# Kernel tuning notes

Hardware: AMD Instinct MI355X
Metric: run time of the kernel (lower is better)

## Reference

```python
import jax, jax.numpy as jnp
import numpy as np

B = 512

def conv2d(x, w, b, stride, pad):
    y = jax.lax.conv_general_dilated(x, w, (stride, stride), [(pad, pad), (pad, pad)],
                                     dimension_numbers=('NCHW', 'OIHW', 'NCHW'))
    return y + b[None, :, None, None]

def maxpool(x, k, s, pad):
    return jax.lax.reduce_window(x, -jnp.inf, jax.lax.max,
                                 (1, 1, k, k), (1, 1, s, s),
                                 [(0, 0), (0, 0), (pad, pad), (pad, pad)])

def squash(s, axis=-1):
    sq = jnp.sum(s * s, axis=axis, keepdims=True)
    return (sq / (1.0 + sq)) * s / jnp.sqrt(sq + 1e-8)

def setup_inputs() -> dict:
    key = jax.random.key(0)
    ks = jax.random.split(key, 24)
    def w(k, shape, fan_in):
        return jax.random.normal(k, shape, dtype=jnp.float32) * np.float32(np.sqrt(2.0 / fan_in))
    inp = {}
    inp['x']  = jax.random.normal(ks[0], (B, 1, 28, 28), dtype=jnp.float32)
    inp['w1'] = w(ks[1], (96, 1, 3, 3), 1 * 9);     inp['b1'] = jnp.zeros((96,), jnp.float32)
    inp['w2'] = w(ks[2], (256, 96, 3, 3), 96 * 9);  inp['b2'] = jnp.zeros((256,), jnp.float32)
    inp['w3'] = w(ks[3], (384, 256, 3, 3), 256 * 9);inp['b3'] = jnp.zeros((384,), jnp.float32)
    inp['w4'] = w(ks[4], (384, 384, 3, 3), 384 * 9);inp['b4'] = jnp.zeros((384,), jnp.float32)
    inp['w5'] = w(ks[5], (256, 384, 3, 3), 384 * 9);inp['b5'] = jnp.zeros((256,), jnp.float32)
    # PrimaryCaps conv: 256 -> 32 caps * 8 dim = 256 channels, k2 s1 p0
    inp['wp'] = w(ks[6], (256, 256, 2, 2), 256 * 4);inp['bp'] = jnp.zeros((256,), jnp.float32)
    # DenseCapsule routing weight [out_caps=10, in_caps=512, out_dim=16, in_dim=8]
    inp['Wr'] = jax.random.normal(ks[7], (10, 512, 16, 8), dtype=jnp.float32) * 0.01
    inp['fw1'] = w(ks[8], (4096, 160), 160);   inp['fb1'] = jnp.zeros((4096,), jnp.float32)
    inp['fw2'] = w(ks[9], (4096, 4096), 4096); inp['fb2'] = jnp.zeros((4096,), jnp.float32)
    inp['fw3'] = w(ks[10], (10, 4096), 4096);  inp['fb3'] = jnp.zeros((10,), jnp.float32)
    return inp

def reference(x, w1, b1, w2, b2, w3, b3, w4, b4, w5, b5, wp, bp, Wr,
              fw1, fb1, fw2, fb2, fw3, fb3):
    # AlexNet-style conv stack (eval mode; dropout = identity)
    h = jax.nn.relu(conv2d(x, w1, b1, 1, 1))   # [B,96,28,28]
    h = maxpool(h, 3, 2, 1)                    # [B,96,14,14]
    h = jax.nn.relu(conv2d(h, w2, b2, 1, 1))   # [B,256,14,14]
    h = maxpool(h, 3, 2, 1)                    # [B,256,7,7]
    h = jax.nn.relu(conv2d(h, w3, b3, 1, 1))   # [B,384,7,7]
    h = jax.nn.relu(conv2d(h, w4, b4, 1, 1))   # [B,384,7,7]
    h = jax.nn.relu(conv2d(h, w5, b5, 1, 1))   # [B,256,7,7]
    h = maxpool(h, 3, 1, 0)                    # [B,256,5,5]
    # PrimaryCaps: conv k2 -> [B,256,4,4] -> [B,512,8] -> squash
    p = conv2d(h, wp, bp, 1, 0)                # [B,256,4,4]
    u = p.reshape(p.shape[0], -1, 8)           # [B,512,8]
    u = squash(u)
    # DenseCapsule dynamic routing (3 iterations)
    x_hat = jnp.einsum('oivd,bid->boiv', Wr, u)     # [B,10,512,16]
    x_hat_d = jax.lax.stop_gradient(x_hat)
    b = jnp.zeros(x_hat.shape[:3], x_hat.dtype)     # [B,10,512]
    routings = 3
    for i in range(routings):
        c = jax.nn.softmax(b, axis=1)
        if i == routings - 1:
            v = squash(jnp.einsum('boi,boiv->bov', c, x_hat))
        else:
            v = squash(jnp.einsum('boi,boiv->bov', c, x_hat_d))
            b = b + jnp.einsum('bov,boiv->boi', v, x_hat_d)
    # Flatten + FC head
    f = v.reshape(v.shape[0], -1)                   # [B,160]
    f = jax.nn.relu(f @ fw1.T + fb1)
    f = jax.nn.relu(f @ fw2.T + fb2)
    return f @ fw3.T + fb3                          # [B,10]
```

## Files before the change

### kernel.cpp

```cpp
#include <hip/hip_runtime.h>
#include <math.h>


#define BATCH 512

typedef _Float16 half8  __attribute__((ext_vector_type(8)));
typedef _Float16 half4v __attribute__((ext_vector_type(4)));
typedef float   float4v __attribute__((ext_vector_type(4)));

__global__ __launch_bounds__(256) void split_kernel(
    const float* __restrict__ src, _Float16* __restrict__ hi,
    _Float16* __restrict__ lo, int n)
{
    int idx = blockIdx.x * 256 + threadIdx.x;
    if (idx >= n) return;
    float v = src[idx];
    _Float16 h = (_Float16)v;
    hi[idx] = h;
    lo[idx] = (_Float16)((v - (float)h) * 2048.0f);
}

__global__ __launch_bounds__(256) void wsplit_nhwc_kernel(
    const float* __restrict__ src, _Float16* __restrict__ hi,
    _Float16* __restrict__ lo, int IC, int KK, int n)
{
    int idx = blockIdx.x * 256 + threadIdx.x;
    if (idx >= n) return;
    int ic   = idx % IC;  int t1 = idx / IC;
    int khkw = t1 % KK;   int oc = t1 / KK;
    float v = src[((size_t)(oc * IC + ic)) * KK + khkw];
    _Float16 h = (_Float16)v;
    hi[idx] = h;
    lo[idx] = (_Float16)((v - (float)h) * 2048.0f);
}

__global__ __launch_bounds__(256) void conv1_pool_nhwc(
    const float* __restrict__ x, const float* __restrict__ w1,
    const float* __restrict__ b1, _Float16* __restrict__ oh_,
    _Float16* __restrict__ ol_)
{
    int idx = blockIdx.x * 256 + threadIdx.x;
    if (idx >= 512 * 14 * 14 * 96) return;
    int oc = idx % 96; int t1 = idx / 96;
    int ow = t1 % 14;  int t2 = t1 / 14;
    int oh = t2 % 14;  int n  = t2 / 14;
    const float* xi = x + n * 784;
    float w[9];
#pragma unroll
    for (int i = 0; i < 9; ++i) w[i] = w1[oc * 9 + i];
    float bias = b1[oc];
    float best = -3.4e38f;
#pragma unroll
    for (int dy = 0; dy < 3; ++dy) {
        int ph = oh * 2 - 1 + dy;
        if ((unsigned)ph >= 28u) continue;
#pragma unroll
        for (int dx = 0; dx < 3; ++dx) {
            int pw = ow * 2 - 1 + dx;
            if ((unsigned)pw >= 28u) continue;
            float s = bias;
#pragma unroll
            for (int ky = 0; ky < 3; ++ky) {
                int iy = ph - 1 + ky;
                if ((unsigned)iy >= 28u) continue;
#pragma unroll
                for (int kx = 0; kx < 3; ++kx) {
                    int ix = pw - 1 + kx;
                    if ((unsigned)ix >= 28u) continue;
                    s = fmaf(w[ky * 3 + kx], xi[iy * 28 + ix], s);
                }
            }
            s = fmaxf(s, 0.f);
            best = fmaxf(best, s);
        }
    }
    _Float16 h = (_Float16)best;
    oh_[idx] = h;
    ol_[idx] = (_Float16)((best - (float)h) * 2048.0f);
}

template<int NB, int C, int H, int W, int OH, int OW, int KS, int STR, int PADP>
__global__ __launch_bounds__(256) void maxpool_nhwc_split(
    const float* __restrict__ in, _Float16* __restrict__ po,
    _Float16* __restrict__ pl)
{
    constexpr int TOTAL = NB * OH * OW * C;
    int idx = blockIdx.x * 256 + threadIdx.x;
    if (idx >= TOTAL) return;
    int c  = idx % C;  int t1 = idx / C;
    int ow = t1 % OW;  int t2 = t1 / OW;
    int oh = t2 % OH;  int n  = t2 / OH;
    const float* ip = in + (size_t)n * (H * W * C) + c;
    float best = -3.4e38f;
#pragma unroll
    for (int dy = 0; dy < KS; ++dy) {
        int ih = oh * STR - PADP + dy;
        if ((unsigned)ih >= (unsigned)H) continue;
#pragma unroll
        for (int dx = 0; dx < KS; ++dx) {
            int iw = ow * STR - PADP + dx;
            if ((unsigned)iw >= (unsigned)W) continue;
            best = fmaxf(best, ip[(size_t)(ih * W + iw) * C]);
        }
    }
    _Float16 h = (_Float16)best;
    po[idx] = h;
    pl[idx] = (_Float16)((best - (float)h) * 2048.0f);
}

template<int IC, int H, int W, int KH, int PAD, int OC, int OUTMODE>
__global__ __launch_bounds__(256, 3) void conv_nhwc_f16x3(
    const _Float16* __restrict__ inh, const _Float16* __restrict__ inl,
    const _Float16* __restrict__ whi, const _Float16* __restrict__ wlo,
    const float* __restrict__ bias,
    float* __restrict__ outf, _Float16* __restrict__ outh,
    _Float16* __restrict__ outl, int n_base)
{
    constexpr int OH  = H + 2 * PAD - KH + 1;
    constexpr int OW  = W + 2 * PAD - KH + 1;
    constexpr int OHW = OH * OW;
    constexpr int K   = IC * KH * KH;
    constexpr int RS  = 40;
    static_assert(IC % 32 == 0, "K-step must sit inside one (kh,kw)");

    const int t    = threadIdx.x;
    const int lane = t & 63;
    const int wid  = t >> 6;
    const int wm   = (wid >> 1) << 6;
    const int wn   = (wid & 1) << 5;
    const int l15  = lane & 15;
    const int quad = lane >> 4;

    __shared__ __align__(16) _Float16 Ah[128 * RS];
    __shared__ __align__(16) _Float16 Al[128 * RS];
    __shared__ __align__(16) _Float16 Bh[64 * RS];
    __shared__ __align__(16) _Float16 Bl[64 * RS];

    const int n0 = blockIdx.x << 6;
    const int m0 = blockIdx.y << 7;

    float4v acc1[8], acc2[8];
#pragma unroll
    for (int i = 0; i < 8; ++i) {
        acc1[i] = (float4v)(0.f);
        acc2[i] = (float4v)(0.f);
    }

    const int am = t >> 1;
    const int ak = (t & 1) << 4;
    const _Float16* wh_p = whi + (size_t)(m0 + am) * K + ak;
    const _Float16* wl_p = wlo + (size_t)(m0 + am) * K + ak;

    const int n_u  = t & 63;
    const int k8   = ((t >> 6) & 3) << 3;
    const int gn_u = n_base + n0 + n_u;
    const int b_u  = gn_u / OHW;
    const int p_u  = gn_u - b_u * OHW;
    const int oh_u = p_u / OW;
    const int ow_u = p_u - oh_u * OW;
    const _Float16* inbh = inh + (size_t)b_u * (H * W * IC);
    const _Float16* inbl = inl + (size_t)b_u * (H * W * IC);

    int khkw = 0, icb = 0;
    for (int kb = 0; kb < K; kb += 32) {
        *(half8*)&Ah[am * RS + ak]     = *(const half8*)(wh_p + kb);
        *(half8*)&Ah[am * RS + ak + 8] = *(const half8*)(wh_p + kb + 8);
        *(half8*)&Al[am * RS + ak]     = *(const half8*)(wl_p + kb);
        *(half8*)&Al[am * RS + ak + 8] = *(const half8*)(wl_p + kb + 8);
        {
            const int kh = khkw / KH;
            const int kw = khkw - kh * KH;
            const int ih = oh_u + kh - PAD;
            const int iw = ow_u + kw - PAD;
            half8 hv = (half8)(_Float16)0.f;
            half8 lv = (half8)(_Float16)0.f;
            if ((unsigned)ih < (unsigned)H && (unsigned)iw < (unsigned)W) {
                const size_t off = (size_t)(ih * W + iw) * IC + icb + k8;
                hv = *(const half8*)(inbh + off);
                lv = *(const half8*)(inbl + off);
            }
            *(half8*)&Bh[n_u * RS + k8] = hv;
            *(half8*)&Bl[n_u * RS + k8] = lv;
        }
        __syncthreads();
        half8 ah[4], al[4], bh[2], bl[2];
#pragma unroll
        for (int i = 0; i < 4; ++i) {
            int ar = wm + i * 16 + l15;
            ah[i] = *(const half8*)&Ah[ar * RS + quad * 8];
            al[i] = *(const half8*)&Al[ar * RS + quad * 8];
        }
#pragma unroll
        for (int i = 0; i < 2; ++i) {
            int br = wn + i * 16 + l15;
            bh[i] = *(const half8*)&Bh[br * RS + quad * 8];
            bl[i] = *(const half8*)&Bl[br * RS + quad * 8];
        }
#pragma unroll
        for (int mi = 0; mi < 4; ++mi)
#pragma unroll
            for (int ni = 0; ni < 2; ++ni) {
                int ix = mi * 2 + ni;
                acc1[ix] = __builtin_amdgcn_mfma_f32_16x16x32_f16(ah[mi], bh[ni], acc1[ix], 0, 0, 0);
                acc2[ix] = __builtin_amdgcn_mfma_f32_16x16x32_f16(ah[mi], bl[ni], acc2[ix], 0, 0, 0);
                acc2[ix] = __builtin_amdgcn_mfma_f32_16x16x32_f16(al[mi], bh[ni], acc2[ix], 0, 0, 0);
            }
        __syncthreads();
        icb += 32;
        if (icb == IC) { icb = 0; ++khkw; }
    }
#pragma unroll
    for (int mi = 0; mi < 4; ++mi)
#pragma unroll
        for (int ni = 0; ni < 2; ++ni) {
            int ix = mi * 2 + ni;
            int gn = n_base + n0 + wn + ni * 16 + l15;
            int ln = gn - n_base;
            int mb = m0 + wm + mi * 16 + quad * 4;
            float4v bv = *(const float4v*)(bias + mb);
            float vv[4];
#pragma unroll
            for (int r = 0; r < 4; ++r) {
                float v = acc1[ix][r] + acc2[ix][r] * (1.0f / 2048.0f) + bv[r];
                if (OUTMODE != 2) v = fmaxf(v, 0.f);
                vv[r] = v;
            }
            if (OUTMODE == 0) {
                float4v o = {vv[0], vv[1], vv[2], vv[3]};
                *(float4v*)(outf + (size_t)ln * OC + mb) = o;
            } else if (OUTMODE == 1) {
                half4v hh, ll;
#pragma unroll
                for (int r = 0; r < 4; ++r) {
                    _Float16 h = (_Float16)vv[r];
                    hh[r] = h;
                    ll[r] = (_Float16)((vv[r] - (float)h) * 2048.0f);
                }
                *(half4v*)(outh + (size_t)ln * OC + mb) = hh;
                *(half4v*)(outl + (size_t)ln * OC + mb) = ll;
            } else {
                int b = gn / OHW;
                int p = gn - b * OHW;
#pragma unroll
                for (int r = 0; r < 4; ++r)
                    outf[((size_t)b * OC + mb + r) * OHW + p] = vv[r];
            }
        }
}

__global__ __launch_bounds__(256, 2) void fc2_f16x3(
    const _Float16* __restrict__ f1h, const _Float16* __restrict__ f1l,
    const float* __restrict__ Bw, float* __restrict__ part, int kslice)
{
    constexpr int K = 4096, N = 4096;
    constexpr int RS = 40;
    const int t    = threadIdx.x;
    const int lane = t & 63;
    const int wid  = t >> 6;
    const int wm   = (wid >> 1) << 6;
    const int wn   = (wid & 1) << 6;
    const int l15  = lane & 15;
    const int quad = lane >> 4;

    __shared__ __align__(16) _Float16 Ah[128 * RS];
    __shared__ __align__(16) _Float16 Al[128 * RS];
    __shared__ __align__(16) _Float16 Bh[128 * RS];
    __shared__ __align__(16) _Float16 Bl[128 * RS];

    const int n0 = blockIdx.x << 7;
    const int m0 = blockIdx.y << 7;
    const int kbeg = blockIdx.z * kslice;

    float4v acc1[16], acc2[16];
#pragma unroll
    for (int i = 0; i < 16; ++i) {
        acc1[i] = (float4v)(0.f);
        acc2[i] = (float4v)(0.f);
    }

    const int am = t >> 1;
    const int ak = (t & 1) << 4;
    const _Float16* ah_p = f1h + (size_t)(m0 + am) * K + kbeg + ak;
    const _Float16* al_p = f1l + (size_t)(m0 + am) * K + kbeg + ak;
    const float*    bw_p = Bw  + (size_t)(n0 + am) * K + kbeg + ak;

    for (int kb = 0; kb < kslice; kb += 32) {
        *(half8*)&Ah[am * RS + ak]     = *(const half8*)(ah_p + kb);
        *(half8*)&Ah[am * RS + ak + 8] = *(const half8*)(ah_p + kb + 8);
        *(half8*)&Al[am * RS + ak]     = *(const half8*)(al_p + kb);
        *(half8*)&Al[am * RS + ak + 8] = *(const half8*)(al_p + kb + 8);
        {
            half8 hv0, lv0, hv1, lv1;
#pragma unroll
            for (int j = 0; j < 8; ++j) {
                float v = bw_p[kb + j];
                _Float16 h = (_Float16)v;
                hv0[j] = h;
                lv0[j] = (_Float16)((v - (float)h) * 2048.0f);
            }
#pragma unroll
            for (int j = 0; j < 8; ++j) {
                float v = bw_p[kb + 8 + j];
                _Float16 h = (_Float16)v;
                hv1[j] = h;
                lv1[j] = (_Float16)((v - (float)h) * 2048.0f);
            }
            *(half8*)&Bh[am * RS + ak]     = hv0;
            *(half8*)&Bh[am * RS + ak + 8] = hv1;
            *(half8*)&Bl[am * RS + ak]     = lv0;
            *(half8*)&Bl[am * RS + ak + 8] = lv1;
        }
        __syncthreads();
        half8 ah[4], al[4], bh[4], bl[4];
#pragma unroll
        for (int i = 0; i < 4; ++i) {
            int ar = wm + i * 16 + l15;
            int br = wn + i * 16 + l15;
            ah[i] = *(const half8*)&Ah[ar * RS + quad * 8];
            al[i] = *(const half8*)&Al[ar * RS + quad * 8];
            bh[i] = *(const half8*)&Bh[br * RS + quad * 8];
            bl[i] = *(const half8*)&Bl[br * RS + quad * 8];
        }
#pragma unroll
        for (int mi = 0; mi < 4; ++mi)
#pragma unroll
            for (int ni = 0; ni < 4; ++ni) {
                int ix = mi * 4 + ni;
                acc1[ix] = __builtin_amdgcn_mfma_f32_16x16x32_f16(ah[mi], bh[ni], acc1[ix], 0, 0, 0);
                acc2[ix] = __builtin_amdgcn_mfma_f32_16x16x32_f16(ah[mi], bl[ni], acc2[ix], 0, 0, 0);
                acc2[ix] = __builtin_amdgcn_mfma_f32_16x16x32_f16(al[mi], bh[ni], acc2[ix], 0, 0, 0);
            }
        __syncthreads();
    }
    float* po = part + (size_t)blockIdx.z * (512 * 4096);
#pragma unroll
    for (int mi = 0; mi < 4; ++mi)
#pragma unroll
        for (int ni = 0; ni < 4; ++ni) {
            int ix = mi * 4 + ni;
            int gn = n0 + wn + ni * 16 + l15;
#pragma unroll
            for (int r = 0; r < 4; ++r) {
                int m = m0 + wm + mi * 16 + quad * 4 + r;
                po[(size_t)m * N + gn] = acc1[ix][r] + acc2[ix][r] * (1.0f / 2048.0f);
            }
        }
}

__global__ __launch_bounds__(256) void fc2_reduce_kernel(
    const float* __restrict__ part, const float* __restrict__ bias,
    float* __restrict__ out)
{
    int idx = blockIdx.x * 256 + threadIdx.x;
    if (idx >= 512 * 4096) return;
    const size_t MN = (size_t)512 * 4096;
    float s = 0.f;
#pragma unroll
    for (int zz = 0; zz < 4; ++zz) s += part[zz * MN + idx];
    s += bias[idx & 4095];
    out[idx] = fmaxf(s, 0.f);
}

template<bool RELU>
__global__ __launch_bounds__(256) void fc_gemm(
    const float* __restrict__ A, const float* __restrict__ Bw,
    const float* __restrict__ bias, float* __restrict__ out,
    int K, int N)
{
    const int t  = threadIdx.x;
    const int j0 = blockIdx.x << 6;
    const int m0 = blockIdx.y << 7;

    __shared__ __align__(16) float As[16 * 132];
    __shared__ __align__(16) float Bs[16 * 64];

    float acc[8][4];
#pragma unroll
    for (int a = 0; a < 8; ++a)
#pragma unroll
        for (int b = 0; b < 4; ++b) acc[a][b] = 0.f;

    const int a_m  = t >> 2;
    const int a_k  = (t & 3) << 2;
    const int b_j  = t & 63;
    const int b_k0 = (t >> 6) << 2;
    const int ms = (t >> 4) << 3;
    const int js = (t & 15) << 2;

    for (int kb0 = 0; kb0 < K; kb0 += 16) {
#pragma unroll
        for (int r = 0; r < 2; ++r) {
            int m = m0 + a_m + (r << 6);
            float4 av = *(const float4*)(A + (size_t)m * K + kb0 + a_k);
            As[(a_k + 0) * 132 + a_m + (r << 6)] = av.x;
            As[(a_k + 1) * 132 + a_m + (r << 6)] = av.y;
            As[(a_k + 2) * 132 + a_m + (r << 6)] = av.z;
            As[(a_k + 3) * 132 + a_m + (r << 6)] = av.w;
        }
        {
            float4 bv = *(const float4*)(Bw + (size_t)(j0 + b_j) * K + kb0 + b_k0);
            Bs[(b_k0 + 0) * 64 + b_j] = bv.x;
            Bs[(b_k0 + 1) * 64 + b_j] = bv.y;
            Bs[(b_k0 + 2) * 64 + b_j] = bv.z;
            Bs[(b_k0 + 3) * 64 + b_j] = bv.w;
        }
        __syncthreads();
#pragma unroll
        for (int kk = 0; kk < 16; ++kk) {
            float4 A0 = *(const float4*)&As[kk * 132 + ms];
            float4 A1 = *(const float4*)&As[kk * 132 + ms + 4];
            float4 B0 = *(const float4*)&Bs[(kk << 6) + js];
            float av[8] = {A0.x, A0.y, A0.z, A0.w, A1.x, A1.y, A1.z, A1.w};
            float bv[4] = {B0.x, B0.y, B0.z, B0.w};
#pragma unroll
            for (int mm = 0; mm < 8; ++mm)
#pragma unroll
                for (int jj = 0; jj < 4; ++jj)
                    acc[mm][jj] = fmaf(av[mm], bv[jj], acc[mm][jj]);
        }
        __syncthreads();
    }
    float4 b4 = *(const float4*)(bias + j0 + js);
#pragma unroll
    for (int mm = 0; mm < 8; ++mm) {
        float4 o;
        o.x = acc[mm][0] + b4.x;
        o.y = acc[mm][1] + b4.y;
        o.z = acc[mm][2] + b4.z;
        o.w = acc[mm][3] + b4.w;
        if (RELU) {
            o.x = fmaxf(o.x, 0.f); o.y = fmaxf(o.y, 0.f);
            o.z = fmaxf(o.z, 0.f); o.w = fmaxf(o.w, 0.f);
        }
        *(float4*)(out + (size_t)(m0 + ms + mm) * N + j0 + js) = o;
    }
}

__global__ __launch_bounds__(256) void squash_kernel(
    const float* __restrict__ p, float* __restrict__ u)
{
    int cap = blockIdx.x * 256 + threadIdx.x;
    if (cap >= 512 * 512) return;
    const float4* pi = (const float4*)(p + (size_t)cap * 8);
    float4 a = pi[0], b = pi[1];
    float sq = a.x * a.x + a.y * a.y + a.z * a.z + a.w * a.w
             + b.x * b.x + b.y * b.y + b.z * b.z + b.w * b.w;
    float f  = sq / (1.f + sq);
    float rs = sqrtf(sq + 1e-8f);
    float4 o0, o1;
    o0.x = (f * a.x) / rs; o0.y = (f * a.y) / rs;
    o0.z = (f * a.z) / rs; o0.w = (f * a.w) / rs;
    o1.x = (f * b.x) / rs; o1.y = (f * b.y) / rs;
    o1.z = (f * b.z) / rs; o1.w = (f * b.w) / rs;
    float4* po = (float4*)(u + (size_t)cap * 8);
    po[0] = o0; po[1] = o1;
}

__global__ __launch_bounds__(256) void xhat_kernel(
    const float* __restrict__ u,
    const float* __restrict__ Wr,
    float* __restrict__ xh)
{
    const int t  = threadIdx.x;
    const int o  = blockIdx.y;
    const int i0 = blockIdx.x << 5;
    const int ii = t & 31;
    const int bs = t >> 5;

    __shared__ __align__(16) float wsh[32 * 132];

    const float* wsrc = Wr + ((size_t)o * 512 + i0) * 128;
    for (int idx = t; idx < 1024; idx += 256) {
        float4 wv = *(const float4*)(wsrc + idx * 4);
        int r = (idx * 4) >> 7;
        int c = (idx * 4) & 127;
        *(float4*)&wsh[r * 132 + c] = wv;
    }
    __syncthreads();

    const int i = i0 + ii;
    const float* wrow = &wsh[ii * 132];

#pragma unroll
    for (int cch = 0; cch < 4; ++cch) {
        float uu[8][8];
#pragma unroll
        for (int l = 0; l < 8; ++l) {
            int b = bs + (cch << 6) + (l << 3);
            float4 u0 = *(const float4*)(u + (size_t)b * 4096 + i * 8);
            float4 u1 = *(const float4*)(u + (size_t)b * 4096 + i * 8 + 4);
            uu[l][0] = u0.x; uu[l][1] = u0.y; uu[l][2] = u0.z; uu[l][3] = u0.w;
            uu[l][4] = u1.x; uu[l][5] = u1.y; uu[l][6] = u1.z; uu[l][7] = u1.w;
        }
#pragma unroll
        for (int v = 0; v < 16; ++v) {
            float4 w0 = *(const float4*)&wrow[v << 3];
            float4 w1 = *(const float4*)&wrow[(v << 3) + 4];
            float acc[8];
#pragma unroll
            for (int l = 0; l < 8; ++l) {
                acc[l] = uu[l][0] * w0.x + uu[l][1] * w0.y + uu[l][2] * w0.z + uu[l][3] * w0.w
                       + uu[l][4] * w1.x + uu[l][5] * w1.y + uu[l][6] * w1.z + uu[l][7] * w1.w;
            }
#pragma unroll
            for (int l = 0; l < 8; ++l) {
                int b = bs + (cch << 6) + (l << 3);
                xh[(((size_t)(o << 4) + v) * 256 + b) * 512 + i] = acc[l];
            }
        }
    }
}

__global__ __launch_bounds__(256) void routing2_kernel(
    const float* __restrict__ xh,
    float* __restrict__ vout)
{
    const int b = blockIdx.x;
    const int t = threadIdx.x;

    __shared__ __align__(16) float b_s[5120];
    __shared__ __align__(16) float c_s[5120];
    __shared__ float s_s[160];
    __shared__ float v_s[160];

    for (int idx = t; idx < 5120; idx += 256) b_s[idx] = 0.f;
    __syncthreads();

    const int o_t = t >> 4;
    const float* xrow = xh + ((size_t)t * 256 + b) * 512;

    for (int it = 0; it < 3; ++it) {
        for (int i = t; i < 512; i += 256) {
            float bv[10], mx = -3.4e38f;
#pragma unroll
            for (int o = 0; o < 10; ++o) { bv[o] = b_s[(o << 9) + i]; mx = fmaxf(mx, bv[o]); }
            float sum = 0.f;
#pragma unroll
            for (int o = 0; o < 10; ++o) { bv[o] = expf(bv[o] - mx); sum += bv[o]; }
            float inv = 1.f / sum;
#pragma unroll
            for (int o = 0; o < 10; ++o) c_s[(o << 9) + i] = bv[o] * inv;
        }
        __syncthreads();
        if (t < 160) {
            const float* cp = c_s + (o_t << 9);
            float4 a0 = {0.f, 0.f, 0.f, 0.f};
            float4 a1 = {0.f, 0.f, 0.f, 0.f};
            for (int i = 0; i < 512; i += 8) {
                float4 x0 = *(const float4*)(xrow + i);
                float4 x1 = *(const float4*)(xrow + i + 4);
                float4 c0 = *(const float4*)(cp + i);
                float4 c1 = *(const float4*)(cp + i + 4);
                a0.x = fmaf(x0.x, c0.x, a0.x); a0.y = fmaf(x0.y, c0.y, a0.y);
                a0.z = fmaf(x0.z, c0.z, a0.z); a0.w = fmaf(x0.w, c0.w, a0.w);
                a1.x = fmaf(x1.x, c1.x, a1.x); a1.y = fmaf(x1.y, c1.y, a1.y);
                a1.z = fmaf(x1.z, c1.z, a1.z); a1.w = fmaf(x1.w, c1.w, a1.w);
            }
            s_s[t] = (a0.x + a0.y) + (a0.z + a0.w) + (a1.x + a1.y) + (a1.z + a1.w);
        }
        __syncthreads();
        if (t < 10) {
            float tv[16], sq = 0.f;
#pragma unroll
            for (int v = 0; v < 16; ++v) { tv[v] = s_s[(t << 4) + v]; sq = fmaf(tv[v], tv[v], sq); }
            float f  = sq / (1.f + sq);
            float rs = sqrtf(sq + 1e-8f);
#pragma unroll
            for (int v = 0; v < 16; ++v) v_s[(t << 4) + v] = (f * tv[v]) / rs;
        }
        __syncthreads();
        if (it < 2) {
            for (int p = t; p < 5120; p += 256) {
                int o = p >> 9;
                int i = p & 511;
                const float* xp = xh + ((size_t)(o << 4) * 256 + b) * 512 + i;
                float acc = b_s[p];
#pragma unroll
                for (int v = 0; v < 16; ++v)
                    acc = fmaf(v_s[(o << 4) + v], xp[(size_t)v * (256 * 512)], acc);
                b_s[p] = acc;
            }
            __syncthreads();
        }
    }

    for (int idx = t; idx < 160; idx += 256) vout[(size_t)b * 160 + idx] = v_s[idx];
}

__global__ __launch_bounds__(256) void fc3_kernel(
    const float* __restrict__ f, const float* __restrict__ w,
    const float* __restrict__ bias, float* __restrict__ out)
{
    const int n = blockIdx.x;
    const int t = threadIdx.x;
    const int lane = t & 63, wv = t >> 6;
    const float* fr = f + (size_t)n * 4096;
    float p[10];
#pragma unroll
    for (int j = 0; j < 10; ++j) p[j] = 0.f;
    for (int k = t; k < 4096; k += 256) {
        float x = fr[k];
#pragma unroll
        for (int j = 0; j < 10; ++j) p[j] = fmaf(x, w[j * 4096 + k], p[j]);
    }
    __shared__ float red[4 * 10];
#pragma unroll
    for (int j = 0; j < 10; ++j) {
        float x = p[j];
        for (int off = 32; off > 0; off >>= 1) x += __shfl_xor(x, off);
        p[j] = x;
    }
    if (lane == 0) {
#pragma unroll
        for (int j = 0; j < 10; ++j) red[wv * 10 + j] = p[j];
    }
    __syncthreads();
    if (t < 10)
        out[(size_t)n * 10 + t] = red[t] + red[10 + t] + red[20 + t] + red[30 + t] + bias[t];
}

extern "C" void kernel_launch(void* const* d_in, const int* in_sizes, int n_in,
                              void* d_out, int out_size, void* d_ws, size_t ws_size,
                              hipStream_t stream)
{
    const float* x   = (const float*)d_in[0];
    const float* w1  = (const float*)d_in[1];
    const float* b1  = (const float*)d_in[2];
    const float* w2  = (const float*)d_in[3];
    const float* b2  = (const float*)d_in[4];
    const float* w3  = (const float*)d_in[5];
    const float* b3  = (const float*)d_in[6];
    const float* w4  = (const float*)d_in[7];
    const float* b4  = (const float*)d_in[8];
    const float* w5  = (const float*)d_in[9];
    const float* b5  = (const float*)d_in[10];
    const float* wp  = (const float*)d_in[11];
    const float* bp  = (const float*)d_in[12];
    const float* Wr  = (const float*)d_in[13];
    const float* fw1 = (const float*)d_in[14];
    const float* fb1 = (const float*)d_in[15];
    const float* fw2 = (const float*)d_in[16];
    const float* fb2 = (const float*)d_in[17];
    const float* fw3 = (const float*)d_in[18];
    const float* fb3 = (const float*)d_in[19];
    float* outp = (float*)d_out;

    char* w = (char*)d_ws;
    _Float16* w2h  = (_Float16*)(w + 115605504);
    _Float16* w2l  = (_Float16*)(w + 116047872);
    _Float16* w3h  = (_Float16*)(w + 116490240);
    _Float16* w3l  = (_Float16*)(w + 118259712);
    _Float16* w4h  = (_Float16*)(w + 120029184);
    _Float16* w4l  = (_Float16*)(w + 122683392);
    _Float16* w5h  = (_Float16*)(w + 125337600);
    _Float16* w5l  = (_Float16*)(w + 127107072);
    _Float16* wph  = (_Float16*)(w + 128876544);
    _Float16* wpl  = (_Float16*)(w + 129400832);

    _Float16* p1h  = (_Float16*)(w + 0);
    _Float16* p1l  = (_Float16*)(w + 19267584);
    float*    a2   = (float*)(w + 38535168);
    _Float16* p2h  = (_Float16*)(w + 89915392);
    _Float16* p2l  = (_Float16*)(w + 102760448);
    _Float16* a3h  = (_Float16*)(w + 0);
    _Float16* a3l  = (_Float16*)(w + 19267584);
    _Float16* a4h  = (_Float16*)(w + 38535168);
    _Float16* a4l  = (_Float16*)(w + 57802752);
    float*    a5   = (float*)(w + 0);
    _Float16* p3h  = (_Float16*)(w + 25690112);
    _Float16* p3l  = (_Float16*)(w + 32243712);
    float*    pc   = (float*)(w + 0);
    float*    u    = (float*)(w + 8388608);
    float*    vcap = (float*)(w + 16777216);
    float*    xh   = (float*)(w + 17104896);
    float*    f1   = (float*)(w + 17104896);
    _Float16* f1h  = (_Float16*)(w + 25493504);
    _Float16* f1l  = (_Float16*)(w + 29687808);
    float*    part = (float*)(w + 33882112);
    float*    f2   = (float*)(w + 67436544);

    wsplit_nhwc_kernel<<<dim3(864),  dim3(256), 0, stream>>>(w2, w2h, w2l,  96, 9,  221184);
    wsplit_nhwc_kernel<<<dim3(3456), dim3(256), 0, stream>>>(w3, w3h, w3l, 256, 9,  884736);
    wsplit_nhwc_kernel<<<dim3(5184), dim3(256), 0, stream>>>(w4, w4h, w4l, 384, 9, 1327104);
    wsplit_nhwc_kernel<<<dim3(3456), dim3(256), 0, stream>>>(w5, w5h, w5l, 384, 9,  884736);
    wsplit_nhwc_kernel<<<dim3(1024), dim3(256), 0, stream>>>(wp, wph, wpl, 256, 4,  262144);

    conv1_pool_nhwc<<<dim3(37632), dim3(256), 0, stream>>>(x, w1, b1, p1h, p1l);

    conv_nhwc_f16x3<96, 14, 14, 3, 1, 256, 0><<<dim3(784, 2), dim3(256), 0, stream>>>(
        p1h, p1l, w2h, w2l, b2, a2, nullptr, nullptr, 0);
    maxpool_nhwc_split<256, 256, 14, 14, 7, 7, 3, 2, 1><<<dim3(12544), dim3(256), 0, stream>>>(
        a2, p2h, p2l);
    conv_nhwc_f16x3<96, 14, 14, 3, 1, 256, 0><<<dim3(784, 2), dim3(256), 0, stream>>>(
        p1h, p1l, w2h, w2l, b2, a2, nullptr, nullptr, 50176);
    maxpool_nhwc_split<256, 256, 14, 14, 7, 7, 3, 2, 1><<<dim3(12544), dim3(256), 0, stream>>>(
        a2, p2h + (size_t)3211264, p2l + (size_t)3211264);

    conv_nhwc_f16x3<256, 7, 7, 3, 1, 384, 1><<<dim3(392, 3), dim3(256), 0, stream>>>(
        p2h, p2l, w3h, w3l, b3, nullptr, a3h, a3l, 0);
    conv_nhwc_f16x3<384, 7, 7, 3, 1, 384, 1><<<dim3(392, 3), dim3(256), 0, stream>>>(
        a3h, a3l, w4h, w4l, b4, nullptr, a4h, a4l, 0);
    conv_nhwc_f16x3<384, 7, 7, 3, 1, 256, 0><<<dim3(392, 2), dim3(256), 0, stream>>>(
        a4h, a4l, w5h, w5l, b5, a5, nullptr, nullptr, 0);
    maxpool_nhwc_split<512, 256, 7, 7, 5, 5, 3, 1, 0><<<dim3(12800), dim3(256), 0, stream>>>(
        a5, p3h, p3l);
    conv_nhwc_f16x3<256, 5, 5, 2, 0, 256, 2><<<dim3(128, 2), dim3(256), 0, stream>>>(
        p3h, p3l, wph, wpl, bp, pc, nullptr, nullptr, 0);
    squash_kernel<<<dim3(1024), dim3(256), 0, stream>>>(pc, u);

    for (int h = 0; h < 2; ++h) {
        const float* uh = u + (size_t)h * 256 * 4096;
        float* vh = vcap + (size_t)h * 256 * 160;
        xhat_kernel<<<dim3(16, 10), dim3(256), 0, stream>>>(uh, Wr, xh);
        routing2_kernel<<<dim3(256), dim3(256), 0, stream>>>(xh, vh);
    }

    fc_gemm<true><<<dim3(64, 4), dim3(256), 0, stream>>>(vcap, fw1, fb1, f1, 160, 4096);
    split_kernel<<<dim3(8192), dim3(256), 0, stream>>>(f1, f1h, f1l, 2097152);
    fc2_f16x3<<<dim3(32, 4, 4), dim3(256), 0, stream>>>(f1h, f1l, fw2, part, 1024);
    fc2_reduce_kernel<<<dim3(8192), dim3(256), 0, stream>>>(part, fb2, f2);
    fc3_kernel<<<dim3(512), dim3(256), 0, stream>>>(f2, fw3, fb3, outp);
}
```

Measured before the change: 1.721 ms.

## Load conv and FC2 tiles via direct global-to-LDS DMA with swizzled layout

Replaces register-staged tile loads in the implicit-GEMM conv and FC2 kernels with global_load_lds direct-to-LDS transfers into XOR-swizzled 64-wide K tiles. Out-of-bounds im2col reads now point at a shared zero page. Conv N tiles grow to 128 and the K step to 64, with weights padded to a multiple of 64. FC2 weights are pre-split to hi/lo fp16 by a separate kernel instead of being converted inside the GEMM. The aim is to cut VGPR traffic and LDS bank conflicts and to remove in-loop conversion work, at the cost of an extra split pass over the 64 MB fw2, a larger LDS footprint and lower occupancy (launch bounds 2).

```diff
diff --git a/kernel.cpp b/kernel.cpp
--- a/kernel.cpp
+++ b/kernel.cpp
@@ -7,6 +7,19 @@
 typedef _Float16 half8  __attribute__((ext_vector_type(8)));
 typedef _Float16 half4v __attribute__((ext_vector_type(4)));
 typedef float   float4v __attribute__((ext_vector_type(4)));
+
+__device__ __forceinline__ void gload_lds16(const void* g, void* l)
+{
+    __builtin_amdgcn_global_load_lds(
+        (const __attribute__((address_space(1))) unsigned int*)g,
+        (__attribute__((address_space(3))) unsigned int*)l,
+        16, 0, 0);
+}
+
+__global__ __launch_bounds__(64) void zero_kernel(float* __restrict__ z)
+{
+    z[threadIdx.x] = 0.f;
+}
 
 __global__ __launch_bounds__(256) void split_kernel(
     const float* __restrict__ src, _Float16* __restrict__ hi,
@@ -20,15 +33,20 @@
     lo[idx] = (_Float16)((v - (float)h) * 2048.0f);
 }
 
-__global__ __launch_bounds__(256) void wsplit_nhwc_kernel(
+__global__ __launch_bounds__(256) void wsplit_pad_kernel(
     const float* __restrict__ src, _Float16* __restrict__ hi,
-    _Float16* __restrict__ lo, int IC, int KK, int n)
+    _Float16* __restrict__ lo, int IC, int KK, int K, int KP, int total)
 {
     int idx = blockIdx.x * 256 + threadIdx.x;
-    if (idx >= n) return;
-    int ic   = idx % IC;  int t1 = idx / IC;
-    int khkw = t1 % KK;   int oc = t1 / KK;
-    float v = src[((size_t)(oc * IC + ic)) * KK + khkw];
+    if (idx >= total) return;
+    int k  = idx % KP;
+    int oc = idx / KP;
+    float v = 0.f;
+    if (k < K) {
+        int khkw = k / IC;
+        int ic   = k - khkw * IC;
+        v = src[((size_t)(oc * IC + ic)) * KK + khkw];
+    }
     _Float16 h = (_Float16)v;
     hi[idx] = h;
     lo[idx] = (_Float16)((v - (float)h) * 2048.0f);
@@ -108,11 +126,11 @@
     pl[idx] = (_Float16)((best - (float)h) * 2048.0f);
 }
 
-template<int IC, int H, int W, int KH, int PAD, int OC, int OUTMODE>
-__global__ __launch_bounds__(256, 3) void conv_nhwc_f16x3(
+template<int IC, int H, int W, int KH, int PAD, int OC, int NT, int OUTMODE>
+__global__ __launch_bounds__(256, 2) void conv_dma(
     const _Float16* __restrict__ inh, const _Float16* __restrict__ inl,
     const _Float16* __restrict__ whi, const _Float16* __restrict__ wlo,
-    const float* __restrict__ bias,
+    const float* __restrict__ bias, const float* __restrict__ zpage,
     float* __restrict__ outf, _Float16* __restrict__ outh,
     _Float16* __restrict__ outl, int n_base)
 {
@@ -120,103 +138,136 @@
     constexpr int OW  = W + 2 * PAD - KH + 1;
     constexpr int OHW = OH * OW;
     constexpr int K   = IC * KH * KH;
-    constexpr int RS  = 40;
-    static_assert(IC % 32 == 0, "K-step must sit inside one (kh,kw)");
+    constexpr int KP  = (K + 63) & ~63;
+    constexpr int NFRAG = NT / 32;
+    constexpr int NBI   = NT / 32;
+    constexpr bool UNIF = (IC % 64 == 0) && (KP == K);
+    constexpr int HWIC = H * W * IC;
 
     const int t    = threadIdx.x;
     const int lane = t & 63;
     const int wid  = t >> 6;
-    const int wm   = (wid >> 1) << 6;
-    const int wn   = (wid & 1) << 5;
     const int l15  = lane & 15;
     const int quad = lane >> 4;
-
-    __shared__ __align__(16) _Float16 Ah[128 * RS];
-    __shared__ __align__(16) _Float16 Al[128 * RS];
-    __shared__ __align__(16) _Float16 Bh[64 * RS];
-    __shared__ __align__(16) _Float16 Bl[64 * RS];
-
-    const int n0 = blockIdx.x << 6;
+    const int wm   = (wid >> 1) << 6;
+    const int wn   = (wid & 1) * (NT / 2);
+
+    const int drow  = lane >> 3;
+    const int pslot = lane & 7;
+    const int slog  = pslot ^ drow;
+
+    __shared__ __align__(16) _Float16 Ah[128 * 64];
+    __shared__ __align__(16) _Float16 Al[128 * 64];
+    __shared__ __align__(16) _Float16 Bh[NT * 64];
+    __shared__ __align__(16) _Float16 Bl[NT * 64];
+
+    const int n0 = blockIdx.x * NT;
     const int m0 = blockIdx.y << 7;
 
-    float4v acc1[8], acc2[8];
-#pragma unroll
-    for (int i = 0; i < 8; ++i) {
+    float4v acc1[4 * NFRAG], acc2[4 * NFRAG];
+#pragma unroll
+    for (int i = 0; i < 4 * NFRAG; ++i) {
         acc1[i] = (float4v)(0.f);
         acc2[i] = (float4v)(0.f);
     }
 
-    const int am = t >> 1;
-    const int ak = (t & 1) << 4;
-    const _Float16* wh_p = whi + (size_t)(m0 + am) * K + ak;
-    const _Float16* wl_p = wlo + (size_t)(m0 + am) * K + ak;
-
-    const int n_u  = t & 63;
-    const int k8   = ((t >> 6) & 3) << 3;
-    const int gn_u = n_base + n0 + n_u;
-    const int b_u  = gn_u / OHW;
-    const int p_u  = gn_u - b_u * OHW;
-    const int oh_u = p_u / OW;
-    const int ow_u = p_u - oh_u * OW;
-    const _Float16* inbh = inh + (size_t)b_u * (H * W * IC);
-    const _Float16* inbl = inl + (size_t)b_u * (H * W * IC);
+    int bU[NBI], ohU[NBI], owU[NBI];
+#pragma unroll
+    for (int ii = 0; ii < NBI; ++ii) {
+        int nl = ((wid * NBI + ii) << 3) + drow;
+        int gn = n_base + n0 + nl;
+        int b  = gn / OHW;
+        int p  = gn - b * OHW;
+        int o  = p / OW;
+        bU[ii] = b; ohU[ii] = o; owU[ii] = p - o * OW;
+    }
 
     int khkw = 0, icb = 0;
-    for (int kb = 0; kb < K; kb += 32) {
-        *(half8*)&Ah[am * RS + ak]     = *(const half8*)(wh_p + kb);
-        *(half8*)&Ah[am * RS + ak + 8] = *(const half8*)(wh_p + kb + 8);
-        *(half8*)&Al[am * RS + ak]     = *(const half8*)(wl_p + kb);
-        *(half8*)&Al[am * RS + ak + 8] = *(const half8*)(wl_p + kb + 8);
-        {
+    for (int kb = 0; kb < KP; kb += 64) {
+#pragma unroll
+        for (int ii = 0; ii < 4; ++ii) {
+            const int iA = (wid << 2) + ii;
+            const size_t go = (size_t)(m0 + (iA << 3) + drow) * KP + kb + (slog << 3);
+            gload_lds16(whi + go, &Ah[(size_t)iA << 9]);
+            gload_lds16(wlo + go, &Al[(size_t)iA << 9]);
+        }
+        if constexpr (UNIF) {
             const int kh = khkw / KH;
             const int kw = khkw - kh * KH;
-            const int ih = oh_u + kh - PAD;
-            const int iw = ow_u + kw - PAD;
-            half8 hv = (half8)(_Float16)0.f;
-            half8 lv = (half8)(_Float16)0.f;
-            if ((unsigned)ih < (unsigned)H && (unsigned)iw < (unsigned)W) {
-                const size_t off = (size_t)(ih * W + iw) * IC + icb + k8;
-                hv = *(const half8*)(inbh + off);
-                lv = *(const half8*)(inbl + off);
-            }
-            *(half8*)&Bh[n_u * RS + k8] = hv;
-            *(half8*)&Bl[n_u * RS + k8] = lv;
-        }
-        __syncthreads();
-        half8 ah[4], al[4], bh[2], bl[2];
-#pragma unroll
-        for (int i = 0; i < 4; ++i) {
-            int ar = wm + i * 16 + l15;
-            ah[i] = *(const half8*)&Ah[ar * RS + quad * 8];
-            al[i] = *(const half8*)&Al[ar * RS + quad * 8];
-        }
-#pragma unroll
-        for (int i = 0; i < 2; ++i) {
-            int br = wn + i * 16 + l15;
-            bh[i] = *(const half8*)&Bh[br * RS + quad * 8];
-            bl[i] = *(const half8*)&Bl[br * RS + quad * 8];
-        }
-#pragma unroll
-        for (int mi = 0; mi < 4; ++mi)
-#pragma unroll
-            for (int ni = 0; ni < 2; ++ni) {
-                int ix = mi * 2 + ni;
-                acc1[ix] = __builtin_amdgcn_mfma_f32_16x16x32_f16(ah[mi], bh[ni], acc1[ix], 0, 0, 0);
-                acc2[ix] = __builtin_amdgcn_mfma_f32_16x16x32_f16(ah[mi], bl[ni], acc2[ix], 0, 0, 0);
-                acc2[ix] = __builtin_amdgcn_mfma_f32_16x16x32_f16(al[mi], bh[ni], acc2[ix], 0, 0, 0);
-            }
-        __syncthreads();
-        icb += 32;
-        if (icb == IC) { icb = 0; ++khkw; }
+#pragma unroll
+            for (int ii = 0; ii < NBI; ++ii) {
+                const int iB = wid * NBI + ii;
+                const int ih = ohU[ii] + kh - PAD;
+                const int iw = owU[ii] + kw - PAD;
+                const bool ok = ((unsigned)ih < (unsigned)H) && ((unsigned)iw < (unsigned)W);
+                const size_t off = (size_t)bU[ii] * HWIC + (ih * W + iw) * IC + icb + (slog << 3);
+                const _Float16* sh = ok ? inh + off : (const _Float16*)zpage;
+                const _Float16* sl = ok ? inl + off : (const _Float16*)zpage;
+                gload_lds16(sh, &Bh[(size_t)iB << 9]);
+                gload_lds16(sl, &Bl[(size_t)iB << 9]);
+            }
+            icb += 64;
+            if (icb == IC) { icb = 0; ++khkw; }
+        } else {
+            const int kpl = kb + (slog << 3);
+            const int kkl = kpl / IC;
+            const int icl = kpl - kkl * IC;
+            const int khl = kkl / KH;
+            const int kwl = kkl - khl * KH;
+#pragma unroll
+            for (int ii = 0; ii < NBI; ++ii) {
+                const int iB = wid * NBI + ii;
+                const int ih = ohU[ii] + khl - PAD;
+                const int iw = owU[ii] + kwl - PAD;
+                const bool ok = (kpl < K) && ((unsigned)ih < (unsigned)H) &&
+                                ((unsigned)iw < (unsigned)W);
+                const size_t off = (size_t)bU[ii] * HWIC + (ih * W + iw) * IC + icl;
+                const _Float16* sh = ok ? inh + off : (const _Float16*)zpage;
+                const _Float16* sl = ok ? inl + off : (const _Float16*)zpage;
+                gload_lds16(sh, &Bh[(size_t)iB << 9]);
+                gload_lds16(sl, &Bl[(size_t)iB << 9]);
+            }
+        }
+        __syncthreads();
+#pragma unroll
+        for (int kh2 = 0; kh2 < 2; ++kh2) {
+            half8 a_h[4], a_l[4], b_h[NFRAG], b_l[NFRAG];
+#pragma unroll
+            for (int i = 0; i < 4; ++i) {
+                const int r  = wm + (i << 4) + l15;
+                const int sl = ((kh2 << 2) + quad) ^ (r & 7);
+                const int off = (r << 6) + (sl << 3);
+                a_h[i] = *(const half8*)&Ah[off];
+                a_l[i] = *(const half8*)&Al[off];
+            }
+#pragma unroll
+            for (int i = 0; i < NFRAG; ++i) {
+                const int r  = wn + (i << 4) + l15;
+                const int sl = ((kh2 << 2) + quad) ^ (r & 7);
+                const int off = (r << 6) + (sl << 3);
+                b_h[i] = *(const half8*)&Bh[off];
+                b_l[i] = *(const half8*)&Bl[off];
+            }
+#pragma unroll
+            for (int mi = 0; mi < 4; ++mi)
+#pragma unroll
+                for (int ni = 0; ni < NFRAG; ++ni) {
+                    const int ix = mi * NFRAG + ni;
+                    acc1[ix] = __builtin_amdgcn_mfma_f32_16x16x32_f16(a_h[mi], b_h[ni], acc1[ix], 0, 0, 0);
+                    acc2[ix] = __builtin_amdgcn_mfma_f32_16x16x32_f16(a_h[mi], b_l[ni], acc2[ix], 0, 0, 0);
+                    acc2[ix] = __builtin_amdgcn_mfma_f32_16x16x32_f16(a_l[mi], b_h[ni], acc2[ix], 0, 0, 0);
+                }
+        }
+        __syncthreads();
     }
 #pragma unroll
     for (int mi = 0; mi < 4; ++mi)
 #pragma unroll
-        for (int ni = 0; ni < 2; ++ni) {
-            int ix = mi * 2 + ni;
-            int gn = n_base + n0 + wn + ni * 16 + l15;
-            int ln = gn - n_base;
-            int mb = m0 + wm + mi * 16 + quad * 4;
+        for (int ni = 0; ni < NFRAG; ++ni) {
+            const int ix = mi * NFRAG + ni;
+            const int gn = n_base + n0 + wn + (ni << 4) + l15;
+            const int ln = gn - n_base;
+            const int mb = m0 + wm + (mi << 4) + (quad << 2);
             float4v bv = *(const float4v*)(bias + mb);
             float vv[4];
 #pragma unroll
@@ -248,24 +299,28 @@
         }
 }
 
-__global__ __launch_bounds__(256, 2) void fc2_f16x3(
-    const _Float16* __restrict__ f1h, const _Float16* __restrict__ f1l,
-    const float* __restrict__ Bw, float* __restrict__ part, int kslice)
+__global__ __launch_bounds__(256, 2) void fc2_dma(
+    const _Float16* __restrict__ ah_g, const _Float16* __restrict__ al_g,
+    const _Float16* __restrict__ bh_g, const _Float16* __restrict__ bl_g,
+    float* __restrict__ part, int kslice)
 {
     constexpr int K = 4096, N = 4096;
-    constexpr int RS = 40;
     const int t    = threadIdx.x;
     const int lane = t & 63;
     const int wid  = t >> 6;
+    const int l15  = lane & 15;
+    const int quad = lane >> 4;
     const int wm   = (wid >> 1) << 6;
     const int wn   = (wid & 1) << 6;
-    const int l15  = lane & 15;
-    const int quad = lane >> 4;
-
-    __shared__ __align__(16) _Float16 Ah[128 * RS];
-    __shared__ __align__(16) _Float16 Al[128 * RS];
-    __shared__ __align__(16) _Float16 Bh[128 * RS];
-    __shared__ __align__(16) _Float16 Bl[128 * RS];
+
+    const int drow  = lane >> 3;
+    const int pslot = lane & 7;
+    const int slog  = pslot ^ drow;
+
+    __shared__ __align__(16) _Float16 Ah[128 * 64];
+    __shared__ __align__(16) _Float16 Al[128 * 64];
+    __shared__ __align__(16) _Float16 Bh[128 * 64];
+    __shared__ __align__(16) _Float16 Bl[128 * 64];
 
     const int n0 = blockIdx.x << 7;
     const int m0 = blockIdx.y << 7;
@@ -278,58 +333,44 @@
         acc2[i] = (float4v)(0.f);
     }
 
-    const int am = t >> 1;
-    const int ak = (t & 1) << 4;
-    const _Float16* ah_p = f1h + (size_t)(m0 + am) * K + kbeg + ak;
-    const _Float16* al_p = f1l + (size_t)(m0 + am) * K + kbeg + ak;
-    const float*    bw_p = Bw  + (size_t)(n0 + am) * K + kbeg + ak;
-
-    for (int kb = 0; kb < kslice; kb += 32) {
-        *(half8*)&Ah[am * RS + ak]     = *(const half8*)(ah_p + kb);
-        *(half8*)&Ah[am * RS + ak + 8] = *(const half8*)(ah_p + kb + 8);
-        *(half8*)&Al[am * RS + ak]     = *(const half8*)(al_p + kb);
-        *(half8*)&Al[am * RS + ak + 8] = *(const half8*)(al_p + kb + 8);
-        {
-            half8 hv0, lv0, hv1, lv1;
-#pragma unroll
-            for (int j = 0; j < 8; ++j) {
-                float v = bw_p[kb + j];
-                _Float16 h = (_Float16)v;
-                hv0[j] = h;
-                lv0[j] = (_Float16)((v - (float)h) * 2048.0f);
-            }
-#pragma unroll
-            for (int j = 0; j < 8; ++j) {
-                float v = bw_p[kb + 8 + j];
-                _Float16 h = (_Float16)v;
-                hv1[j] = h;
-                lv1[j] = (_Float16)((v - (float)h) * 2048.0f);
-            }
-            *(half8*)&Bh[am * RS + ak]     = hv0;
-            *(half8*)&Bh[am * RS + ak + 8] = hv1;
-            *(half8*)&Bl[am * RS + ak]     = lv0;
-            *(half8*)&Bl[am * RS + ak + 8] = lv1;
-        }
-        __syncthreads();
-        half8 ah[4], al[4], bh[4], bl[4];
-#pragma unroll
-        for (int i = 0; i < 4; ++i) {
-            int ar = wm + i * 16 + l15;
-            int br = wn + i * 16 + l15;
-            ah[i] = *(const half8*)&Ah[ar * RS + quad * 8];
-            al[i] = *(const half8*)&Al[ar * RS + quad * 8];
-            bh[i] = *(const half8*)&Bh[br * RS + quad * 8];
-            bl[i] = *(const half8*)&Bl[br * RS + quad * 8];
-        }
-#pragma unroll
-        for (int mi = 0; mi < 4; ++mi)
-#pragma unroll
-            for (int ni = 0; ni < 4; ++ni) {
-                int ix = mi * 4 + ni;
-                acc1[ix] = __builtin_amdgcn_mfma_f32_16x16x32_f16(ah[mi], bh[ni], acc1[ix], 0, 0, 0);
-                acc2[ix] = __builtin_amdgcn_mfma_f32_16x16x32_f16(ah[mi], bl[ni], acc2[ix], 0, 0, 0);
-                acc2[ix] = __builtin_amdgcn_mfma_f32_16x16x32_f16(al[mi], bh[ni], acc2[ix], 0, 0, 0);
-            }
+    for (int kb = 0; kb < kslice; kb += 64) {
+#pragma unroll
+        for (int ii = 0; ii < 4; ++ii) {
+            const int iA = (wid << 2) + ii;
+            const size_t ga = (size_t)(m0 + (iA << 3) + drow) * K + kbeg + kb + (slog << 3);
+            gload_lds16(ah_g + ga, &Ah[(size_t)iA << 9]);
+            gload_lds16(al_g + ga, &Al[(size_t)iA << 9]);
+            const size_t gb = (size_t)(n0 + (iA << 3) + drow) * K + kbeg + kb + (slog << 3);
+            gload_lds16(bh_g + gb, &Bh[(size_t)iA << 9]);
+            gload_lds16(bl_g + gb, &Bl[(size_t)iA << 9]);
+        }
+        __syncthreads();
+#pragma unroll
+        for (int kh2 = 0; kh2 < 2; ++kh2) {
+            half8 a_h[4], a_l[4], b_h[4], b_l[4];
+#pragma unroll
+            for (int i = 0; i < 4; ++i) {
+                const int ra  = wm + (i << 4) + l15;
+                const int sa  = ((kh2 << 2) + quad) ^ (ra & 7);
+                const int oa  = (ra << 6) + (sa << 3);
+                a_h[i] = *(const half8*)&Ah[oa];
+                a_l[i] = *(const half8*)&Al[oa];
+                const int rb  = wn + (i << 4) + l15;
+                const int sb  = ((kh2 << 2) + quad) ^ (rb & 7);
+                const int ob  = (rb << 6) + (sb << 3);
+                b_h[i] = *(const half8*)&Bh[ob];
+                b_l[i] = *(const half8*)&Bl[ob];
+            }
+#pragma unroll
+            for (int mi = 0; mi < 4; ++mi)
+#pragma unroll
+                for (int ni = 0; ni < 4; ++ni) {
+                    const int ix = mi * 4 + ni;
+                    acc1[ix] = __builtin_amdgcn_mfma_f32_16x16x32_f16(a_h[mi], b_h[ni], acc1[ix], 0, 0, 0);
+                    acc2[ix] = __builtin_amdgcn_mfma_f32_16x16x32_f16(a_h[mi], b_l[ni], acc2[ix], 0, 0, 0);
+                    acc2[ix] = __builtin_amdgcn_mfma_f32_16x16x32_f16(a_l[mi], b_h[ni], acc2[ix], 0, 0, 0);
+                }
+        }
         __syncthreads();
     }
     float* po = part + (size_t)blockIdx.z * (512 * 4096);
@@ -337,11 +378,11 @@
     for (int mi = 0; mi < 4; ++mi)
 #pragma unroll
         for (int ni = 0; ni < 4; ++ni) {
-            int ix = mi * 4 + ni;
-            int gn = n0 + wn + ni * 16 + l15;
+            const int ix = mi * 4 + ni;
+            const int gn = n0 + wn + (ni << 4) + l15;
 #pragma unroll
             for (int r = 0; r < 4; ++r) {
-                int m = m0 + wm + mi * 16 + quad * 4 + r;
+                const int m = m0 + wm + (mi << 4) + (quad << 2) + r;
                 po[(size_t)m * N + gn] = acc1[ix][r] + acc2[ix][r] * (1.0f / 2048.0f);
             }
         }
@@ -647,15 +688,16 @@
 
     char* w = (char*)d_ws;
     _Float16* w2h  = (_Float16*)(w + 115605504);
-    _Float16* w2l  = (_Float16*)(w + 116047872);
-    _Float16* w3h  = (_Float16*)(w + 116490240);
-    _Float16* w3l  = (_Float16*)(w + 118259712);
-    _Float16* w4h  = (_Float16*)(w + 120029184);
-    _Float16* w4l  = (_Float16*)(w + 122683392);
-    _Float16* w5h  = (_Float16*)(w + 125337600);
-    _Float16* w5l  = (_Float16*)(w + 127107072);
-    _Float16* wph  = (_Float16*)(w + 128876544);
-    _Float16* wpl  = (_Float16*)(w + 129400832);
+    _Float16* w2l  = (_Float16*)(w + 116064256);
+    _Float16* w3h  = (_Float16*)(w + 116523008);
+    _Float16* w3l  = (_Float16*)(w + 118292480);
+    _Float16* w4h  = (_Float16*)(w + 120061952);
+    _Float16* w4l  = (_Float16*)(w + 122716160);
+    _Float16* w5h  = (_Float16*)(w + 125370368);
+    _Float16* w5l  = (_Float16*)(w + 127139840);
+    _Float16* wph  = (_Float16*)(w + 128909312);
+    _Float16* wpl  = (_Float16*)(w + 129433600);
+    float*    zp   = (float*)(w + 129957888);
 
     _Float16* p1h  = (_Float16*)(w + 0);
     _Float16* p1l  = (_Float16*)(w + 19267584);
@@ -673,39 +715,43 @@
     float*    u    = (float*)(w + 8388608);
     float*    vcap = (float*)(w + 16777216);
     float*    xh   = (float*)(w + 17104896);
+
     float*    f1   = (float*)(w + 17104896);
-    _Float16* f1h  = (_Float16*)(w + 25493504);
-    _Float16* f1l  = (_Float16*)(w + 29687808);
-    float*    part = (float*)(w + 33882112);
-    float*    f2   = (float*)(w + 67436544);
-
-    wsplit_nhwc_kernel<<<dim3(864),  dim3(256), 0, stream>>>(w2, w2h, w2l,  96, 9,  221184);
-    wsplit_nhwc_kernel<<<dim3(3456), dim3(256), 0, stream>>>(w3, w3h, w3l, 256, 9,  884736);
-    wsplit_nhwc_kernel<<<dim3(5184), dim3(256), 0, stream>>>(w4, w4h, w4l, 384, 9, 1327104);
-    wsplit_nhwc_kernel<<<dim3(3456), dim3(256), 0, stream>>>(w5, w5h, w5l, 384, 9,  884736);
-    wsplit_nhwc_kernel<<<dim3(1024), dim3(256), 0, stream>>>(wp, wph, wpl, 256, 4,  262144);
+    _Float16* fw2h = (_Float16*)(w + 33882112);
+    _Float16* fw2l = (_Float16*)(w + 67436544);
+    _Float16* f1h  = (_Float16*)(w + 100990976);
+    _Float16* f1l  = (_Float16*)(w + 105185280);
+    float*    part = (float*)(w + 0);
+    float*    f2   = (float*)(w + 33882112);
+
+    zero_kernel<<<dim3(1), dim3(64), 0, stream>>>(zp);
+    wsplit_pad_kernel<<<dim3(896),  dim3(256), 0, stream>>>(w2, w2h, w2l,  96, 9,  864,  896,  229376);
+    wsplit_pad_kernel<<<dim3(3456), dim3(256), 0, stream>>>(w3, w3h, w3l, 256, 9, 2304, 2304,  884736);
+    wsplit_pad_kernel<<<dim3(5184), dim3(256), 0, stream>>>(w4, w4h, w4l, 384, 9, 3456, 3456, 1327104);
+    wsplit_pad_kernel<<<dim3(3456), dim3(256), 0, stream>>>(w5, w5h, w5l, 384, 9, 3456, 3456,  884736);
+    wsplit_pad_kernel<<<dim3(1024), dim3(256), 0, stream>>>(wp, wph, wpl, 256, 4, 1024, 1024,  262144);
 
     conv1_pool_nhwc<<<dim3(37632), dim3(256), 0, stream>>>(x, w1, b1, p1h, p1l);
 
-    conv_nhwc_f16x3<96, 14, 14, 3, 1, 256, 0><<<dim3(784, 2), dim3(256), 0, stream>>>(
-        p1h, p1l, w2h, w2l, b2, a2, nullptr, nullptr, 0);
+    conv_dma<96, 14, 14, 3, 1, 256, 128, 0><<<dim3(392, 2), dim3(256), 0, stream>>>(
+        p1h, p1l, w2h, w2l, b2, zp, a2, nullptr, nullptr, 0);
     maxpool_nhwc_split<256, 256, 14, 14, 7, 7, 3, 2, 1><<<dim3(12544), dim3(256), 0, stream>>>(
         a2, p2h, p2l);
-    conv_nhwc_f16x3<96, 14, 14, 3, 1, 256, 0><<<dim3(784, 2), dim3(256), 0, stream>>>(
-        p1h, p1l, w2h, w2l, b2, a2, nullptr, nullptr, 50176);
+    conv_dma<96, 14, 14, 3, 1, 256, 128, 0><<<dim3(392, 2), dim3(256), 0, stream>>>(
+        p1h, p1l, w2h, w2l, b2, zp, a2, nullptr, nullptr, 50176);
     maxpool_nhwc_split<256, 256, 14, 14, 7, 7, 3, 2, 1><<<dim3(12544), dim3(256), 0, stream>>>(
         a2, p2h + (size_t)3211264, p2l + (size_t)3211264);
 
-    conv_nhwc_f16x3<256, 7, 7, 3, 1, 384, 1><<<dim3(392, 3), dim3(256), 0, stream>>>(
-        p2h, p2l, w3h, w3l, b3, nullptr, a3h, a3l, 0);
-    conv_nhwc_f16x3<384, 7, 7, 3, 1, 384, 1><<<dim3(392, 3), dim3(256), 0, stream>>>(
-        a3h, a3l, w4h, w4l, b4, nullptr, a4h, a4l, 0);
-    conv_nhwc_f16x3<384, 7, 7, 3, 1, 256, 0><<<dim3(392, 2), dim3(256), 0, stream>>>(
-        a4h, a4l, w5h, w5l, b5, a5, nullptr, nullptr, 0);
+    conv_dma<256, 7, 7, 3, 1, 384, 128, 1><<<dim3(196, 3), dim3(256), 0, stream>>>(
+        p2h, p2l, w3h, w3l, b3, zp, nullptr, a3h, a3l, 0);
+    conv_dma<384, 7, 7, 3, 1, 384, 128, 1><<<dim3(196, 3), dim3(256), 0, stream>>>(
+        a3h, a3l, w4h, w4l, b4, zp, nullptr, a4h, a4l, 0);
+    conv_dma<384, 7, 7, 3, 1, 256, 128, 0><<<dim3(196, 2), dim3(256), 0, stream>>>(
+        a4h, a4l, w5h, w5l, b5, zp, a5, nullptr, nullptr, 0);
     maxpool_nhwc_split<512, 256, 7, 7, 5, 5, 3, 1, 0><<<dim3(12800), dim3(256), 0, stream>>>(
         a5, p3h, p3l);
-    conv_nhwc_f16x3<256, 5, 5, 2, 0, 256, 2><<<dim3(128, 2), dim3(256), 0, stream>>>(
-        p3h, p3l, wph, wpl, bp, pc, nullptr, nullptr, 0);
+    conv_dma<256, 5, 5, 2, 0, 256, 64, 2><<<dim3(128, 2), dim3(256), 0, stream>>>(
+        p3h, p3l, wph, wpl, bp, zp, pc, nullptr, nullptr, 0);
     squash_kernel<<<dim3(1024), dim3(256), 0, stream>>>(pc, u);
 
     for (int h = 0; h < 2; ++h) {
@@ -715,9 +761,11 @@
         routing2_kernel<<<dim3(256), dim3(256), 0, stream>>>(xh, vh);
     }
 
+    split_kernel<<<dim3(65536), dim3(256), 0, stream>>>(fw2, fw2h, fw2l, 16777216);
+
     fc_gemm<true><<<dim3(64, 4), dim3(256), 0, stream>>>(vcap, fw1, fb1, f1, 160, 4096);
     split_kernel<<<dim3(8192), dim3(256), 0, stream>>>(f1, f1h, f1l, 2097152);
-    fc2_f16x3<<<dim3(32, 4, 4), dim3(256), 0, stream>>>(f1h, f1l, fw2, part, 1024);
+    fc2_dma<<<dim3(32, 4, 4), dim3(256), 0, stream>>>(f1h, f1l, fw2h, fw2l, part, 1024);
     fc2_reduce_kernel<<<dim3(8192), dim3(256), 0, stream>>>(part, fb2, f2);
     fc3_kernel<<<dim3(512), dim3(256), 0, stream>>>(f2, fw3, fb3, outp);
 }
```

Result: faster. 1.403 ms (-18.5%).
